# Kernel tuning notes

Measured on AMD Instinct MI355X. Metric: run time of the kernel, lower is better.

Reference implementation:

```python
import jax, jax.numpy as jnp
import numpy as np

N_NODES = 100000

def _spmm(edge_index, edge_weight, support):
    # out[dst] += w * support[src]  == sparse adj @ support
    src, dst = edge_index[0], edge_index[1]
    msgs = support[src] * edge_weight[:, None]
    return jax.ops.segment_sum(msgs, dst, num_segments=N_NODES)


def setup_inputs() -> dict:
    key = jax.random.key(0)
    k1, k2, k3, k4, k5 = jax.random.split(key, 5)
    n_feat, n_hid, n_class = 512, 256, 40
    E = 3200000
    x = jax.random.normal(k1, (N_NODES, n_feat), dtype=jnp.float32)
    edge_index = jax.random.randint(k2, (2, E), 0, N_NODES, dtype=jnp.int64)
    edge_weight = jax.random.uniform(k3, (E,), dtype=jnp.float32)
    # Xavier-uniform-like init
    lim1 = float(np.sqrt(6.0 / (n_feat + n_hid)))
    lim2 = float(np.sqrt(6.0 / (n_hid + n_class)))
    W1 = jax.random.uniform(k4, (n_feat, n_hid), minval=-lim1, maxval=lim1, dtype=jnp.float32)
    W2 = jax.random.uniform(k5, (n_hid, n_class), minval=-lim2, maxval=lim2, dtype=jnp.float32)
    return {"x": x, "edge_index": edge_index, "edge_weight": edge_weight, "W1": W1, "W2": W2}


def reference(x, edge_index, edge_weight, W1, W2):
    # layer 1: dense projection then sparse aggregation, relu
    h = jax.nn.relu(_spmm(edge_index, edge_weight, x @ W1))
    # dropout is identity in eval mode (deterministic reference)
    # layer 2
    logits = _spmm(edge_index, edge_weight, h @ W2)
    return jax.nn.log_softmax(logits, axis=1)
```

## Files before the change

kernel.cpp:

```cpp
#include <hip/hip_runtime.h>
#include <math.h>

#define N_FEAT 512
#define F_HID  256
#define F_OUT  40
#define P_STRIDE 64

#define NBLK1 128
#define CAP   224

typedef unsigned short u16;
typedef unsigned int   u32;
typedef unsigned char  u8;
typedef __attribute__((ext_vector_type(8))) short bf8_t;
typedef __attribute__((ext_vector_type(4))) float f32x4;
typedef __attribute__((ext_vector_type(2))) float f32x2;

__device__ __forceinline__ u16 f2bf(float f) {
    unsigned u = __float_as_uint(f);
    u += 0x7FFFu + ((u >> 16) & 1u);
    return (u16)(u >> 16);
}
__device__ __forceinline__ float bf2f(u16 h) {
    return __uint_as_float(((unsigned)h) << 16);
}
__device__ __forceinline__ float bfLo(u32 u) { return __uint_as_float(u << 16); }
__device__ __forceinline__ float bfHi(u32 u) { return __uint_as_float(u & 0xFFFF0000u); }

__global__ void prep_weights(const float* __restrict__ W1, const float* __restrict__ W2,
                             u16* __restrict__ W1T, u16* __restrict__ W2T) {
    int idx = blockIdx.x * blockDim.x + threadIdx.x;
    if (idx < F_HID * N_FEAT) {
        int n = idx >> 9, k = idx & 511;
        W1T[idx] = f2bf(W1[k * F_HID + n]);
    }
    int idx2 = idx - F_HID * N_FEAT;
    if (idx2 >= 0 && idx2 < 48 * 256) {
        int n = idx2 >> 8, k = idx2 & 255;
        W2T[idx2] = (n < F_OUT) ? f2bf(W2[k * F_OUT + n]) : (u16)0;
    }
}

__global__ __launch_bounds__(256) void bucket_kernel(const int* __restrict__ src,
                                                     const int* __restrict__ dst,
                                                     const float* __restrict__ w,
                                                     int2* __restrict__ region,
                                                     int* __restrict__ cnt_g,
                                                     int E, int NB) {
    __shared__ int cnt[256];
    int tid = threadIdx.x;
    cnt[tid] = 0;
    __syncthreads();
    int2* myreg = region + (size_t)blockIdx.x * NB * CAP;
    for (int i = blockIdx.x * 256 + tid; i < E; i += NBLK1 * 256) {
        int d = dst[i];
        int b = d >> 9;
        int pos = atomicAdd(&cnt[b], 1);
        if (pos < CAP)
            myreg[(size_t)b * CAP + pos] =
                make_int2((d & 511) | (src[i] << 9), __float_as_int(w[i]));
    }
    __syncthreads();
    if (tid < NB) cnt_g[blockIdx.x * NB + tid] = min(cnt[tid], CAP);
}

__global__ __launch_bounds__(256) void bucket_scan(const int* __restrict__ cnt_g,
                                                   int* __restrict__ Bb, int NB) {
    __shared__ int t[256];
    int tid = threadIdx.x;
    int T = 0;
    if (tid < NB)
        for (int blk = 0; blk < NBLK1; ++blk) T += cnt_g[blk * NB + tid];
    t[tid] = T;
    __syncthreads();
    for (int d = 1; d < 256; d <<= 1) {
        int v = (tid >= d) ? t[tid - d] : 0;
        __syncthreads();
        t[tid] += v;
        __syncthreads();
    }
    if (tid < NB) Bb[tid] = t[tid] - T;
}

__global__ __launch_bounds__(256) void build_csr(const int2* __restrict__ region,
                                                 const int* __restrict__ cnt_g,
                                                 const int* __restrict__ Bb,
                                                 int* __restrict__ deg,
                                                 int* __restrict__ offs,
                                                 int2* __restrict__ edges,
                                                 int M, int NB) {
    int b = blockIdx.x, tid = threadIdx.x;
    __shared__ int hist[512], excl[512], curi[512], pc[NBLK1];
    __shared__ int s1[256];
    hist[tid] = 0; hist[tid + 256] = 0;
    for (int t = tid; t < NBLK1; t += 256) pc[t] = cnt_g[t * NB + b];
    __syncthreads();
    for (int blk = 0; blk < NBLK1; ++blk) {
        int n = pc[blk];
        const int2* rp = region + ((size_t)blk * NB + b) * CAP;
        for (int j = tid; j < n; j += 256)
            atomicAdd(&hist[rp[j].x & 511], 1);
    }
    __syncthreads();
    int h0 = hist[2 * tid], h1 = hist[2 * tid + 1];
    s1[tid] = h0 + h1;
    __syncthreads();
    for (int d = 1; d < 256; d <<= 1) {
        int v = (tid >= d) ? s1[tid - d] : 0;
        __syncthreads();
        s1[tid] += v;
        __syncthreads();
    }
    int ex = s1[tid] - (h0 + h1);
    excl[2 * tid] = ex;       excl[2 * tid + 1] = ex + h0;
    curi[2 * tid] = ex;       curi[2 * tid + 1] = ex + h0;
    __syncthreads();
    int base = Bb[b];
    for (int t = tid; t < 512; t += 256) {
        int d = b * 512 + t;
        if (d < M) { deg[d] = hist[t]; offs[d] = base + excl[t]; }
    }
    for (int blk = 0; blk < NBLK1; ++blk) {
        int n = pc[blk];
        const int2* rp = region + ((size_t)blk * NB + b) * CAP;
        for (int j = tid; j < n; j += 256) {
            int2 e = rp[j];
            int ld = e.x & 511;
            int p = atomicAdd(&curi[ld], 1);
            edges[base + p] = make_int2(e.x >> 9, e.y);
        }
    }
}

__global__ __launch_bounds__(256) void gemm1_kernel(const float* __restrict__ X,
                                                    const u16* __restrict__ W1T,
                                                    u8* __restrict__ H0, int M) {
    __shared__ float As[2][2048];
    int tid  = threadIdx.x;
    int wv   = tid >> 6, lane = tid & 63;
    int l15  = lane & 15, quad = lane >> 4;
    int m0   = blockIdx.x * 64;

    int p16_0 = wv * 64 + lane;
    int p16_1 = 256 + wv * 64 + lane;
    int r0 = p16_0 >> 3, sc0 = (p16_0 & 7) ^ (r0 & 7);
    int r1 = p16_1 >> 3, sc1 = (p16_1 & 7) ^ (r1 & 7);
    const float* src0 = X + (size_t)min(m0 + r0, M - 1) * N_FEAT + sc0 * 4;
    const float* src1 = X + (size_t)min(m0 + r1, M - 1) * N_FEAT + sc1 * 4;

    f32x4 acc[4][4] = {};

    auto stage = [&](int c, int buf) {
        __builtin_amdgcn_global_load_lds(
            (const __attribute__((address_space(1))) void*)(src0 + c * 32),
            (__attribute__((address_space(3))) void*)(&As[buf][wv * 256]), 16, 0, 0);
        __builtin_amdgcn_global_load_lds(
            (const __attribute__((address_space(1))) void*)(src1 + c * 32),
            (__attribute__((address_space(3))) void*)(&As[buf][1024 + wv * 256]), 16, 0, 0);
    };

    stage(0, 0);
    __syncthreads();
    for (int c = 0; c < 16; ++c) {
        int cur = c & 1;
        if (c + 1 < 16) stage(c + 1, cur ^ 1);
        bf8_t b[4];
#pragma unroll
        for (int nt = 0; nt < 4; ++nt)
            b[nt] = *(const bf8_t*)(W1T + (size_t)(wv * 64 + nt * 16 + l15) * N_FEAT + c * 32 + quad * 8);
#pragma unroll
        for (int mt = 0; mt < 4; ++mt) {
            int m = mt * 16 + l15;
            int scA = (quad * 2) ^ (m & 7);
            int scB = (quad * 2 + 1) ^ (m & 7);
            f32x4 x0 = *(const f32x4*)(&As[cur][m * 32 + scA * 4]);
            f32x4 x1 = *(const f32x4*)(&As[cur][m * 32 + scB * 4]);
            bf8_t a;
            a[0] = (short)f2bf(x0[0]); a[1] = (short)f2bf(x0[1]);
            a[2] = (short)f2bf(x0[2]); a[3] = (short)f2bf(x0[3]);
            a[4] = (short)f2bf(x1[0]); a[5] = (short)f2bf(x1[1]);
            a[6] = (short)f2bf(x1[2]); a[7] = (short)f2bf(x1[3]);
#pragma unroll
            for (int nt = 0; nt < 4; ++nt)
                acc[mt][nt] = __builtin_amdgcn_mfma_f32_16x16x32_bf16(a, b[nt], acc[mt][nt], 0, 0, 0);
        }
        __syncthreads();
    }
#pragma unroll
    for (int mt = 0; mt < 4; ++mt)
#pragma unroll
        for (int nt = 0; nt < 4; ++nt)
#pragma unroll
            for (int r = 0; r < 4; ++r) {
                int row = m0 + mt * 16 + quad * 4 + r;
                if (row < M) {
                    int pk = __builtin_amdgcn_cvt_pk_fp8_f32(acc[mt][nt][r], 0.f, 0, false);
                    H0[(size_t)row * F_HID + wv * 64 + nt * 16 + l15] = (u8)(pk & 0xFF);
                }
            }
}

__global__ __launch_bounds__(256) void spmm1_kernel(const u8* __restrict__ H0,
                                                    const int* __restrict__ offs,
                                                    const int* __restrict__ deg,
                                                    const int2* __restrict__ edges,
                                                    u16* __restrict__ H1, int M) {
    __shared__ int2 sE[4][64];
    int wv = threadIdx.x >> 6, lane = threadIdx.x & 63;
    int d = blockIdx.x * 4 + wv;
    if (d >= M) return;
    int start = offs[d], cnt = deg[d];
    int q = lane >> 4, l16 = lane & 15;
    const u8* hp = H0 + l16 * 16;
    float acc[16] = {};
    for (int base = 0; base < cnt; base += 64) {
        int c = min(64, cnt - base);
        int2 ev = make_int2(0, 0);
        if (lane < c) ev = edges[start + base + lane];
        sE[wv][lane] = ev;
        int jt = (c + 31) >> 5;
        for (int j = 0; j < jt; ++j) {
            int2 e[8];
#pragma unroll
            for (int k = 0; k < 8; ++k)
                e[k] = sE[wv][32 * j + 4 * k + q];
            uint4 v[8];
#pragma unroll
            for (int k = 0; k < 8; ++k)
                v[k] = *(const uint4*)(hp + (size_t)e[k].x * F_HID);
#pragma unroll
            for (int k = 0; k < 8; ++k) {
                float w = __int_as_float(e[k].y);
                u32 wd[4] = {v[k].x, v[k].y, v[k].z, v[k].w};
#pragma unroll
                for (int t = 0; t < 4; ++t) {
                    f32x2 lo = __builtin_amdgcn_cvt_pk_f32_fp8((int)wd[t], false);
                    f32x2 hi = __builtin_amdgcn_cvt_pk_f32_fp8((int)wd[t], true);
                    acc[4 * t + 0] = fmaf(w, lo[0], acc[4 * t + 0]);
                    acc[4 * t + 1] = fmaf(w, lo[1], acc[4 * t + 1]);
                    acc[4 * t + 2] = fmaf(w, hi[0], acc[4 * t + 2]);
                    acc[4 * t + 3] = fmaf(w, hi[1], acc[4 * t + 3]);
                }
            }
        }
    }
#pragma unroll
    for (int t = 0; t < 16; ++t) {
        acc[t] += __shfl_xor(acc[t], 16);
        acc[t] += __shfl_xor(acc[t], 32);
    }
    if (q == 0) {
        u16 o[16];
#pragma unroll
        for (int t = 0; t < 16; ++t) o[t] = f2bf(fmaxf(acc[t], 0.f));
        uint4 r0, r1;
        r0.x = (u32)o[0]  | ((u32)o[1]  << 16);
        r0.y = (u32)o[2]  | ((u32)o[3]  << 16);
        r0.z = (u32)o[4]  | ((u32)o[5]  << 16);
        r0.w = (u32)o[6]  | ((u32)o[7]  << 16);
        r1.x = (u32)o[8]  | ((u32)o[9]  << 16);
        r1.y = (u32)o[10] | ((u32)o[11] << 16);
        r1.z = (u32)o[12] | ((u32)o[13] << 16);
        r1.w = (u32)o[14] | ((u32)o[15] << 16);
        uint4* dst16 = (uint4*)(H1 + (size_t)d * F_HID + l16 * 16);
        dst16[0] = r0;
        dst16[1] = r1;
    }
}

__global__ __launch_bounds__(256) void gemm2_kernel(const u16* __restrict__ H1,
                                                    const u16* __restrict__ W2T,
                                                    u16* __restrict__ P, int M) {
    __shared__ u16 Bs[2][8192];
    int tid  = threadIdx.x;
    int wv   = tid >> 6, lane = tid & 63;
    int l15  = lane & 15, quad = lane >> 4;
    int m0   = blockIdx.x * 128;

    f32x4 acc[2][3] = {};

    auto stage = [&](int c, int buf) {
#pragma unroll
        for (int jj = 0; jj < 4; ++jj) {
            int p16 = jj * 256 + wv * 64 + lane;
            int r   = p16 >> 3;
            int sc  = (p16 & 7) ^ (r & 7);
            const u16* src = H1 + (size_t)min(m0 + r, M - 1) * F_HID + c * 64 + sc * 8;
            __builtin_amdgcn_global_load_lds(
                (const __attribute__((address_space(1))) void*)src,
                (__attribute__((address_space(3))) void*)(&Bs[buf][jj * 2048 + wv * 512]), 16, 0, 0);
        }
    };

    stage(0, 0);
    __syncthreads();
    for (int c = 0; c < 4; ++c) {
        int cur = c & 1;
        if (c + 1 < 4) stage(c + 1, cur ^ 1);
#pragma unroll
        for (int ks = 0; ks < 2; ++ks) {
            bf8_t b[3];
#pragma unroll
            for (int nt = 0; nt < 3; ++nt)
                b[nt] = *(const bf8_t*)(W2T + (size_t)(nt * 16 + l15) * F_HID + c * 64 + ks * 32 + quad * 8);
#pragma unroll
            for (int mt = 0; mt < 2; ++mt) {
                int m  = wv * 32 + mt * 16 + l15;
                int sc = (ks * 4 + quad) ^ (m & 7);
                bf8_t a = *(const bf8_t*)(&Bs[cur][m * 64 + sc * 8]);
#pragma unroll
                for (int nt = 0; nt < 3; ++nt)
                    acc[mt][nt] = __builtin_amdgcn_mfma_f32_16x16x32_bf16(a, b[nt], acc[mt][nt], 0, 0, 0);
            }
        }
        __syncthreads();
    }
#pragma unroll
    for (int mt = 0; mt < 2; ++mt)
#pragma unroll
        for (int nt = 0; nt < 3; ++nt)
#pragma unroll
            for (int r = 0; r < 4; ++r) {
                int row = m0 + wv * 32 + mt * 16 + quad * 4 + r;
                int col = nt * 16 + l15;
                if (row < M && col < F_OUT)
                    P[(size_t)row * P_STRIDE + col] = f2bf(acc[mt][nt][r]);
            }
}

__global__ __launch_bounds__(256) void spmm2_kernel(const u16* __restrict__ P,
                                                    const int* __restrict__ offs,
                                                    const int* __restrict__ deg,
                                                    const int2* __restrict__ edges,
                                                    float* __restrict__ out, int M) {
    __shared__ int2 sE[4][64];
    int wv = threadIdx.x >> 6, lane = threadIdx.x & 63;
    int d = blockIdx.x * 4 + wv;
    if (d >= M) return;
    int start = offs[d], cnt = deg[d];
    int q = lane >> 4, l16 = lane & 15;
    const u16* pp = P + l16 * 4;
    float acc[4] = {};
    for (int base = 0; base < cnt; base += 64) {
        int c = min(64, cnt - base);
        int2 ev = make_int2(0, 0);
        if (lane < c) ev = edges[start + base + lane];
        sE[wv][lane] = ev;
        int jt = (c + 31) >> 5;
        for (int j = 0; j < jt; ++j) {
            int2 e[8];
#pragma unroll
            for (int k = 0; k < 8; ++k)
                e[k] = sE[wv][32 * j + 4 * k + q];
            uint2 v[8];
#pragma unroll
            for (int k = 0; k < 8; ++k)
                v[k] = *(const uint2*)(pp + (size_t)e[k].x * P_STRIDE);
#pragma unroll
            for (int k = 0; k < 8; ++k) {
                float w = __int_as_float(e[k].y);
                acc[0] = fmaf(w, bfLo(v[k].x), acc[0]); acc[1] = fmaf(w, bfHi(v[k].x), acc[1]);
                acc[2] = fmaf(w, bfLo(v[k].y), acc[2]); acc[3] = fmaf(w, bfHi(v[k].y), acc[3]);
            }
        }
    }
#pragma unroll
    for (int t = 0; t < 4; ++t) {
        acc[t] += __shfl_xor(acc[t], 16);
        acc[t] += __shfl_xor(acc[t], 32);
    }
    int fbase = l16 * 4;
    float mx = -INFINITY;
#pragma unroll
    for (int t = 0; t < 4; ++t)
        if (fbase + t < F_OUT) mx = fmaxf(mx, acc[t]);
#pragma unroll
    for (int off = 8; off >= 1; off >>= 1) mx = fmaxf(mx, __shfl_xor(mx, off));
    float sm = 0.f;
#pragma unroll
    for (int t = 0; t < 4; ++t)
        if (fbase + t < F_OUT) sm += expf(acc[t] - mx);
#pragma unroll
    for (int off = 8; off >= 1; off >>= 1) sm += __shfl_xor(sm, off);
    if (q == 0 && l16 < 10) {
        float lse = mx + logf(sm);
        f32x4 o;
#pragma unroll
        for (int t = 0; t < 4; ++t) o[t] = acc[t] - lse;
        *(f32x4*)(out + (size_t)d * F_OUT + fbase) = o;
    }
}

extern "C" void kernel_launch(void* const* d_in, const int* in_sizes, int n_in,
                              void* d_out, int out_size, void* d_ws, size_t ws_size,
                              hipStream_t stream) {
    const float* x   = (const float*)d_in[0];
    const int*   eix = (const int*)d_in[1];
    const float* ewt = (const float*)d_in[2];
    const float* W1  = (const float*)d_in[3];
    const float* W2  = (const float*)d_in[4];
    float* out = (float*)d_out;

    const int E = in_sizes[2];
    const int M = out_size / F_OUT;
    const int NB = (M + 511) >> 9;
    const int* src = eix;
    const int* dst = eix + E;

    char* ws = (char*)d_ws;
    size_t off = 0;
    auto take = [&](size_t bytes) -> void* {
        void* p = ws + off;
        off = (off + bytes + 255) & ~(size_t)255;
        return p;
    };
    u8*    H0     = (u8*)take((size_t)M * F_HID * sizeof(u8));
    u16*   H1     = (u16*)take((size_t)M * F_HID * sizeof(u16));
    u16*   W1T    = (u16*)take((size_t)F_HID * N_FEAT * sizeof(u16));
    u16*   W2T    = (u16*)take((size_t)48 * 256 * sizeof(u16));
    u16*   P      = (u16*)take((size_t)M * P_STRIDE * sizeof(u16));
    int*   deg    = (int*)take((size_t)M * sizeof(int));
    int*   offs   = (int*)take((size_t)M * sizeof(int));
    int*   Bb     = (int*)take(256 * sizeof(int));
    int*   cnt_g  = (int*)take((size_t)NBLK1 * NB * sizeof(int));
    int2*  edges  = (int2*)take((size_t)E * sizeof(int2));
    int2*  region = (int2*)take((size_t)NBLK1 * NB * CAP * sizeof(int2));
    (void)ws_size; (void)n_in;

    int prep_n = F_HID * N_FEAT + 48 * 256;
    prep_weights<<<(prep_n + 255) / 256, 256, 0, stream>>>(W1, W2, W1T, W2T);

    bucket_kernel<<<NBLK1, 256, 0, stream>>>(src, dst, ewt, region, cnt_g, E, NB);
    bucket_scan<<<1, 256, 0, stream>>>(cnt_g, Bb, NB);
    build_csr<<<NB, 256, 0, stream>>>(region, cnt_g, Bb, deg, offs, edges, M, NB);

    gemm1_kernel<<<(M + 63) / 64, 256, 0, stream>>>(x, W1T, H0, M);
    spmm1_kernel<<<(M + 3) / 4, 256, 0, stream>>>(H0, offs, deg, edges, H1, M);
    gemm2_kernel<<<(M + 127) / 128, 256, 0, stream>>>(H1, W2T, P, M);
    spmm2_kernel<<<(M + 3) / 4, 256, 0, stream>>>(P, offs, deg, edges, out, M);
}
```

Baseline: 732.6 us.

## Build CSR via global atomics count-scan-scatter and store layer-2 projection as fp8

Replaces the capped bucket-region CSR build with a global degree count, a multi-block prefix scan, and an atomic-cursor scatter. This removes the per-block capacity limit and the large region buffer, but issues global atomics on random destinations and leaves edge order within each row nondeterministic. The layer-2 projection P is stored as fp8 instead of bf16, halving gather bytes in spmm2. spmm2 is remapped so 8 lanes each cover 8 features, with tail-edge guards added to both spmm kernels.

```diff
diff --git a/kernel.cpp b/kernel.cpp
--- a/kernel.cpp
+++ b/kernel.cpp
@@ -4,10 +4,6 @@
 #define N_FEAT 512
 #define F_HID  256
 #define F_OUT  40
-#define P_STRIDE 64
-
-#define NBLK1 128
-#define CAP   224
 
 typedef unsigned short u16;
 typedef unsigned int   u32;
@@ -21,14 +17,12 @@
     u += 0x7FFFu + ((u >> 16) & 1u);
     return (u16)(u >> 16);
 }
-__device__ __forceinline__ float bf2f(u16 h) {
-    return __uint_as_float(((unsigned)h) << 16);
-}
 __device__ __forceinline__ float bfLo(u32 u) { return __uint_as_float(u << 16); }
 __device__ __forceinline__ float bfHi(u32 u) { return __uint_as_float(u & 0xFFFF0000u); }
 
 __global__ void prep_weights(const float* __restrict__ W1, const float* __restrict__ W2,
-                             u16* __restrict__ W1T, u16* __restrict__ W2T) {
+                             u16* __restrict__ W1T, u16* __restrict__ W2T,
+                             int* __restrict__ deg, int M) {
     int idx = blockIdx.x * blockDim.x + threadIdx.x;
     if (idx < F_HID * N_FEAT) {
         int n = idx >> 9, k = idx & 511;
@@ -39,96 +33,79 @@
         int n = idx2 >> 8, k = idx2 & 255;
         W2T[idx2] = (n < F_OUT) ? f2bf(W2[k * F_OUT + n]) : (u16)0;
     }
-}
-
-__global__ __launch_bounds__(256) void bucket_kernel(const int* __restrict__ src,
-                                                     const int* __restrict__ dst,
-                                                     const float* __restrict__ w,
-                                                     int2* __restrict__ region,
-                                                     int* __restrict__ cnt_g,
-                                                     int E, int NB) {
-    __shared__ int cnt[256];
-    int tid = threadIdx.x;
-    cnt[tid] = 0;
-    __syncthreads();
-    int2* myreg = region + (size_t)blockIdx.x * NB * CAP;
-    for (int i = blockIdx.x * 256 + tid; i < E; i += NBLK1 * 256) {
-        int d = dst[i];
-        int b = d >> 9;
-        int pos = atomicAdd(&cnt[b], 1);
-        if (pos < CAP)
-            myreg[(size_t)b * CAP + pos] =
-                make_int2((d & 511) | (src[i] << 9), __float_as_int(w[i]));
-    }
-    __syncthreads();
-    if (tid < NB) cnt_g[blockIdx.x * NB + tid] = min(cnt[tid], CAP);
-}
-
-__global__ __launch_bounds__(256) void bucket_scan(const int* __restrict__ cnt_g,
-                                                   int* __restrict__ Bb, int NB) {
+    if (idx < M) deg[idx] = 0;
+}
+
+__global__ __launch_bounds__(256) void count_kernel(const int* __restrict__ dst,
+                                                    int* __restrict__ deg, int E) {
+    int i = blockIdx.x * 256 + threadIdx.x;
+    int stride = gridDim.x * 256;
+    for (; i < E; i += stride) atomicAdd(&deg[dst[i]], 1);
+}
+
+__global__ __launch_bounds__(256) void scan_bsum(const int* __restrict__ deg,
+                                                 int* __restrict__ bsum, int M) {
+    __shared__ int s[256];
+    int b = blockIdx.x, tid = threadIdx.x;
+    int i0 = b * 512;
+    int v = 0;
+    if (i0 + tid < M) v += deg[i0 + tid];
+    if (i0 + 256 + tid < M) v += deg[i0 + 256 + tid];
+    s[tid] = v; __syncthreads();
+    for (int d = 128; d > 0; d >>= 1) {
+        if (tid < d) s[tid] += s[tid + d];
+        __syncthreads();
+    }
+    if (tid == 0) bsum[b] = s[0];
+}
+
+__global__ __launch_bounds__(256) void scan_bbase(const int* __restrict__ bsum,
+                                                  int* __restrict__ bbase, int NB) {
     __shared__ int t[256];
     int tid = threadIdx.x;
-    int T = 0;
-    if (tid < NB)
-        for (int blk = 0; blk < NBLK1; ++blk) T += cnt_g[blk * NB + tid];
-    t[tid] = T;
-    __syncthreads();
+    int v = (tid < NB) ? bsum[tid] : 0;
+    t[tid] = v; __syncthreads();
     for (int d = 1; d < 256; d <<= 1) {
-        int v = (tid >= d) ? t[tid - d] : 0;
-        __syncthreads();
-        t[tid] += v;
-        __syncthreads();
-    }
-    if (tid < NB) Bb[tid] = t[tid] - T;
-}
-
-__global__ __launch_bounds__(256) void build_csr(const int2* __restrict__ region,
-                                                 const int* __restrict__ cnt_g,
-                                                 const int* __restrict__ Bb,
-                                                 int* __restrict__ deg,
+        int u = (tid >= d) ? t[tid - d] : 0;
+        __syncthreads();
+        t[tid] += u;
+        __syncthreads();
+    }
+    if (tid < NB) bbase[tid] = t[tid] - v;
+}
+
+__global__ __launch_bounds__(256) void scan_offs(const int* __restrict__ deg,
+                                                 const int* __restrict__ bbase,
                                                  int* __restrict__ offs,
-                                                 int2* __restrict__ edges,
-                                                 int M, int NB) {
+                                                 int* __restrict__ cursor, int M) {
+    __shared__ int s1[256];
     int b = blockIdx.x, tid = threadIdx.x;
-    __shared__ int hist[512], excl[512], curi[512], pc[NBLK1];
-    __shared__ int s1[256];
-    hist[tid] = 0; hist[tid + 256] = 0;
-    for (int t = tid; t < NBLK1; t += 256) pc[t] = cnt_g[t * NB + b];
-    __syncthreads();
-    for (int blk = 0; blk < NBLK1; ++blk) {
-        int n = pc[blk];
-        const int2* rp = region + ((size_t)blk * NB + b) * CAP;
-        for (int j = tid; j < n; j += 256)
-            atomicAdd(&hist[rp[j].x & 511], 1);
-    }
-    __syncthreads();
-    int h0 = hist[2 * tid], h1 = hist[2 * tid + 1];
-    s1[tid] = h0 + h1;
-    __syncthreads();
+    int i0 = b * 512;
+    int d0 = (i0 + 2 * tid < M) ? deg[i0 + 2 * tid] : 0;
+    int d1 = (i0 + 2 * tid + 1 < M) ? deg[i0 + 2 * tid + 1] : 0;
+    s1[tid] = d0 + d1; __syncthreads();
     for (int d = 1; d < 256; d <<= 1) {
-        int v = (tid >= d) ? s1[tid - d] : 0;
-        __syncthreads();
-        s1[tid] += v;
-        __syncthreads();
-    }
-    int ex = s1[tid] - (h0 + h1);
-    excl[2 * tid] = ex;       excl[2 * tid + 1] = ex + h0;
-    curi[2 * tid] = ex;       curi[2 * tid + 1] = ex + h0;
-    __syncthreads();
-    int base = Bb[b];
-    for (int t = tid; t < 512; t += 256) {
-        int d = b * 512 + t;
-        if (d < M) { deg[d] = hist[t]; offs[d] = base + excl[t]; }
-    }
-    for (int blk = 0; blk < NBLK1; ++blk) {
-        int n = pc[blk];
-        const int2* rp = region + ((size_t)blk * NB + b) * CAP;
-        for (int j = tid; j < n; j += 256) {
-            int2 e = rp[j];
-            int ld = e.x & 511;
-            int p = atomicAdd(&curi[ld], 1);
-            edges[base + p] = make_int2(e.x >> 9, e.y);
-        }
+        int u = (tid >= d) ? s1[tid - d] : 0;
+        __syncthreads();
+        s1[tid] += u;
+        __syncthreads();
+    }
+    int ex = s1[tid] - (d0 + d1) + bbase[b];
+    if (i0 + 2 * tid < M)     { offs[i0 + 2 * tid] = ex;      cursor[i0 + 2 * tid] = ex; }
+    if (i0 + 2 * tid + 1 < M) { offs[i0 + 2 * tid + 1] = ex + d0; cursor[i0 + 2 * tid + 1] = ex + d0; }
+}
+
+__global__ __launch_bounds__(256) void scatter_kernel(const int* __restrict__ src,
+                                                      const int* __restrict__ dst,
+                                                      const float* __restrict__ w,
+                                                      int* __restrict__ cursor,
+                                                      int2* __restrict__ edges, int E) {
+    int i = blockIdx.x * 256 + threadIdx.x;
+    int stride = gridDim.x * 256;
+    for (; i < E; i += stride) {
+        int d = dst[i];
+        int p = atomicAdd(&cursor[d], 1);
+        edges[p] = make_int2(src[i], __float_as_int(w[i]));
     }
 }
 
@@ -230,16 +207,18 @@
                 v[k] = *(const uint4*)(hp + (size_t)e[k].x * F_HID);
 #pragma unroll
             for (int k = 0; k < 8; ++k) {
-                float w = __int_as_float(e[k].y);
-                u32 wd[4] = {v[k].x, v[k].y, v[k].z, v[k].w};
-#pragma unroll
-                for (int t = 0; t < 4; ++t) {
-                    f32x2 lo = __builtin_amdgcn_cvt_pk_f32_fp8((int)wd[t], false);
-                    f32x2 hi = __builtin_amdgcn_cvt_pk_f32_fp8((int)wd[t], true);
-                    acc[4 * t + 0] = fmaf(w, lo[0], acc[4 * t + 0]);
-                    acc[4 * t + 1] = fmaf(w, lo[1], acc[4 * t + 1]);
-                    acc[4 * t + 2] = fmaf(w, hi[0], acc[4 * t + 2]);
-                    acc[4 * t + 3] = fmaf(w, hi[1], acc[4 * t + 3]);
+                if (32 * j + 4 * k < c) {
+                    float w = __int_as_float(e[k].y);
+                    u32 wd[4] = {v[k].x, v[k].y, v[k].z, v[k].w};
+#pragma unroll
+                    for (int t = 0; t < 4; ++t) {
+                        f32x2 lo = __builtin_amdgcn_cvt_pk_f32_fp8((int)wd[t], false);
+                        f32x2 hi = __builtin_amdgcn_cvt_pk_f32_fp8((int)wd[t], true);
+                        acc[4 * t + 0] = fmaf(w, lo[0], acc[4 * t + 0]);
+                        acc[4 * t + 1] = fmaf(w, lo[1], acc[4 * t + 1]);
+                        acc[4 * t + 2] = fmaf(w, hi[0], acc[4 * t + 2]);
+                        acc[4 * t + 3] = fmaf(w, hi[1], acc[4 * t + 3]);
+                    }
                 }
             }
         }
@@ -270,7 +249,7 @@
 
 __global__ __launch_bounds__(256) void gemm2_kernel(const u16* __restrict__ H1,
                                                     const u16* __restrict__ W2T,
-                                                    u16* __restrict__ P, int M) {
+                                                    u8* __restrict__ P, int M) {
     __shared__ u16 Bs[2][8192];
     int tid  = threadIdx.x;
     int wv   = tid >> 6, lane = tid & 63;
@@ -323,12 +302,22 @@
             for (int r = 0; r < 4; ++r) {
                 int row = m0 + wv * 32 + mt * 16 + quad * 4 + r;
                 int col = nt * 16 + l15;
-                if (row < M && col < F_OUT)
-                    P[(size_t)row * P_STRIDE + col] = f2bf(acc[mt][nt][r]);
+                if (row < M) {
+                    u8 val = 0;
+                    if (col < F_OUT) {
+                        int pk = __builtin_amdgcn_cvt_pk_fp8_f32(acc[mt][nt][r], 0.f, 0, false);
+                        val = (u8)(pk & 0xFF);
+                    }
+                    P[(size_t)row * 64 + col] = val;
+                }
             }
-}
-
-__global__ __launch_bounds__(256) void spmm2_kernel(const u16* __restrict__ P,
+    for (int rr = tid; rr < 128; rr += 256) {
+        int row = m0 + rr;
+        if (row < M) *(uint4*)(P + (size_t)row * 64 + 48) = make_uint4(0, 0, 0, 0);
+    }
+}
+
+__global__ __launch_bounds__(256) void spmm2_kernel(const u8* __restrict__ P,
                                                     const int* __restrict__ offs,
                                                     const int* __restrict__ deg,
                                                     const int2* __restrict__ edges,
@@ -338,56 +327,65 @@
     int d = blockIdx.x * 4 + wv;
     if (d >= M) return;
     int start = offs[d], cnt = deg[d];
-    int q = lane >> 4, l16 = lane & 15;
-    const u16* pp = P + l16 * 4;
-    float acc[4] = {};
+    int g = lane >> 3, l8 = lane & 7;
+    const u8* pp = P + l8 * 8;
+    float acc[8] = {};
     for (int base = 0; base < cnt; base += 64) {
         int c = min(64, cnt - base);
         int2 ev = make_int2(0, 0);
         if (lane < c) ev = edges[start + base + lane];
         sE[wv][lane] = ev;
-        int jt = (c + 31) >> 5;
-        for (int j = 0; j < jt; ++j) {
-            int2 e[8];
-#pragma unroll
-            for (int k = 0; k < 8; ++k)
-                e[k] = sE[wv][32 * j + 4 * k + q];
-            uint2 v[8];
-#pragma unroll
-            for (int k = 0; k < 8; ++k)
-                v[k] = *(const uint2*)(pp + (size_t)e[k].x * P_STRIDE);
-#pragma unroll
-            for (int k = 0; k < 8; ++k) {
+        int2 e[8];
+#pragma unroll
+        for (int k = 0; k < 8; ++k)
+            e[k] = sE[wv][8 * k + g];
+        uint2 v[8];
+#pragma unroll
+        for (int k = 0; k < 8; ++k)
+            v[k] = *(const uint2*)(pp + (size_t)e[k].x * 64);
+#pragma unroll
+        for (int k = 0; k < 8; ++k) {
+            if (8 * k < c) {
                 float w = __int_as_float(e[k].y);
-                acc[0] = fmaf(w, bfLo(v[k].x), acc[0]); acc[1] = fmaf(w, bfHi(v[k].x), acc[1]);
-                acc[2] = fmaf(w, bfLo(v[k].y), acc[2]); acc[3] = fmaf(w, bfHi(v[k].y), acc[3]);
+                f32x2 lo0 = __builtin_amdgcn_cvt_pk_f32_fp8((int)v[k].x, false);
+                f32x2 hi0 = __builtin_amdgcn_cvt_pk_f32_fp8((int)v[k].x, true);
+                f32x2 lo1 = __builtin_amdgcn_cvt_pk_f32_fp8((int)v[k].y, false);
+                f32x2 hi1 = __builtin_amdgcn_cvt_pk_f32_fp8((int)v[k].y, true);
+                acc[0] = fmaf(w, lo0[0], acc[0]); acc[1] = fmaf(w, lo0[1], acc[1]);
+                acc[2] = fmaf(w, hi0[0], acc[2]); acc[3] = fmaf(w, hi0[1], acc[3]);
+                acc[4] = fmaf(w, lo1[0], acc[4]); acc[5] = fmaf(w, lo1[1], acc[5]);
+                acc[6] = fmaf(w, hi1[0], acc[6]); acc[7] = fmaf(w, hi1[1], acc[7]);
             }
         }
     }
 #pragma unroll
-    for (int t = 0; t < 4; ++t) {
+    for (int t = 0; t < 8; ++t) {
+        acc[t] += __shfl_xor(acc[t], 8);
         acc[t] += __shfl_xor(acc[t], 16);
         acc[t] += __shfl_xor(acc[t], 32);
     }
-    int fbase = l16 * 4;
     float mx = -INFINITY;
-#pragma unroll
-    for (int t = 0; t < 4; ++t)
-        if (fbase + t < F_OUT) mx = fmaxf(mx, acc[t]);
-#pragma unroll
-    for (int off = 8; off >= 1; off >>= 1) mx = fmaxf(mx, __shfl_xor(mx, off));
+    if (l8 < 5) {
+#pragma unroll
+        for (int t = 0; t < 8; ++t) mx = fmaxf(mx, acc[t]);
+    }
+#pragma unroll
+    for (int off = 4; off >= 1; off >>= 1) mx = fmaxf(mx, __shfl_xor(mx, off));
     float sm = 0.f;
-#pragma unroll
-    for (int t = 0; t < 4; ++t)
-        if (fbase + t < F_OUT) sm += expf(acc[t] - mx);
-#pragma unroll
-    for (int off = 8; off >= 1; off >>= 1) sm += __shfl_xor(sm, off);
-    if (q == 0 && l16 < 10) {
+    if (l8 < 5) {
+#pragma unroll
+        for (int t = 0; t < 8; ++t) sm += expf(acc[t] - mx);
+    }
+#pragma unroll
+    for (int off = 4; off >= 1; off >>= 1) sm += __shfl_xor(sm, off);
+    if (g == 0 && l8 < 5) {
         float lse = mx + logf(sm);
-        f32x4 o;
-#pragma unroll
-        for (int t = 0; t < 4; ++t) o[t] = acc[t] - lse;
-        *(f32x4*)(out + (size_t)d * F_OUT + fbase) = o;
+        f32x4 o0, o1;
+#pragma unroll
+        for (int t = 0; t < 4; ++t) { o0[t] = acc[t] - lse; o1[t] = acc[4 + t] - lse; }
+        f32x4* op = (f32x4*)(out + (size_t)d * F_OUT + l8 * 8);
+        op[0] = o0;
+        op[1] = o1;
     }
 }
 
@@ -418,21 +416,24 @@
     u16*   H1     = (u16*)take((size_t)M * F_HID * sizeof(u16));
     u16*   W1T    = (u16*)take((size_t)F_HID * N_FEAT * sizeof(u16));
     u16*   W2T    = (u16*)take((size_t)48 * 256 * sizeof(u16));
-    u16*   P      = (u16*)take((size_t)M * P_STRIDE * sizeof(u16));
+    u8*    P      = (u8*)take((size_t)M * 64 * sizeof(u8));
     int*   deg    = (int*)take((size_t)M * sizeof(int));
     int*   offs   = (int*)take((size_t)M * sizeof(int));
-    int*   Bb     = (int*)take(256 * sizeof(int));
-    int*   cnt_g  = (int*)take((size_t)NBLK1 * NB * sizeof(int));
+    int*   cursor = (int*)take((size_t)M * sizeof(int));
+    int*   bsum   = (int*)take(256 * sizeof(int));
+    int*   bbase  = (int*)take(256 * sizeof(int));
     int2*  edges  = (int2*)take((size_t)E * sizeof(int2));
-    int2*  region = (int2*)take((size_t)NBLK1 * NB * CAP * sizeof(int2));
     (void)ws_size; (void)n_in;
 
     int prep_n = F_HID * N_FEAT + 48 * 256;
-    prep_weights<<<(prep_n + 255) / 256, 256, 0, stream>>>(W1, W2, W1T, W2T);
-
-    bucket_kernel<<<NBLK1, 256, 0, stream>>>(src, dst, ewt, region, cnt_g, E, NB);
-    bucket_scan<<<1, 256, 0, stream>>>(cnt_g, Bb, NB);
-    build_csr<<<NB, 256, 0, stream>>>(region, cnt_g, Bb, deg, offs, edges, M, NB);
+    int prep_grid = (max(prep_n, M) + 255) / 256;
+    prep_weights<<<prep_grid, 256, 0, stream>>>(W1, W2, W1T, W2T, deg, M);
+
+    count_kernel<<<2048, 256, 0, stream>>>(dst, deg, E);
+    scan_bsum<<<NB, 256, 0, stream>>>(deg, bsum, M);
+    scan_bbase<<<1, 256, 0, stream>>>(bsum, bbase, NB);
+    scan_offs<<<NB, 256, 0, stream>>>(deg, bbase, offs, cursor, M);
+    scatter_kernel<<<2048, 256, 0, stream>>>(src, dst, ewt, cursor, edges, E);
 
     gemm1_kernel<<<(M + 63) / 64, 256, 0, stream>>>(x, W1T, H0, M);
     spmm1_kernel<<<(M + 3) / 4, 256, 0, stream>>>(H0, offs, deg, edges, H1, M);
```

Measured after the change: 911.1 us. 24.4% more time.

## Store layer-2 projection as FP8 and regroup SpMM2 gather lanes

Applied to the files above, without the earlier changes.

The gemm2 output P moves from bf16 at stride 64 to fp8 at stride 64 bytes. This halves the bytes gathered per edge in spmm2, which now maps 8 lanes × 8 features so each wave processes 8 edges per step instead of 4. The spmm1 and spmm2 inner loops also skip FMAs for padded edge slots beyond the chunk count. The trade-off is more quantization error in the logits before log_softmax, plus a byte-wise scattered store in gemm2.

```diff
diff --git a/kernel.cpp b/kernel.cpp
--- a/kernel.cpp
+++ b/kernel.cpp
@@ -4,7 +4,6 @@
 #define N_FEAT 512
 #define F_HID  256
 #define F_OUT  40
-#define P_STRIDE 64
 
 #define NBLK1 128
 #define CAP   224
@@ -20,9 +19,6 @@
     unsigned u = __float_as_uint(f);
     u += 0x7FFFu + ((u >> 16) & 1u);
     return (u16)(u >> 16);
-}
-__device__ __forceinline__ float bf2f(u16 h) {
-    return __uint_as_float(((unsigned)h) << 16);
 }
 __device__ __forceinline__ float bfLo(u32 u) { return __uint_as_float(u << 16); }
 __device__ __forceinline__ float bfHi(u32 u) { return __uint_as_float(u & 0xFFFF0000u); }
@@ -230,16 +226,18 @@
                 v[k] = *(const uint4*)(hp + (size_t)e[k].x * F_HID);
 #pragma unroll
             for (int k = 0; k < 8; ++k) {
-                float w = __int_as_float(e[k].y);
-                u32 wd[4] = {v[k].x, v[k].y, v[k].z, v[k].w};
-#pragma unroll
-                for (int t = 0; t < 4; ++t) {
-                    f32x2 lo = __builtin_amdgcn_cvt_pk_f32_fp8((int)wd[t], false);
-                    f32x2 hi = __builtin_amdgcn_cvt_pk_f32_fp8((int)wd[t], true);
-                    acc[4 * t + 0] = fmaf(w, lo[0], acc[4 * t + 0]);
-                    acc[4 * t + 1] = fmaf(w, lo[1], acc[4 * t + 1]);
-                    acc[4 * t + 2] = fmaf(w, hi[0], acc[4 * t + 2]);
-                    acc[4 * t + 3] = fmaf(w, hi[1], acc[4 * t + 3]);
+                if (32 * j + 4 * k < c) {
+                    float w = __int_as_float(e[k].y);
+                    u32 wd[4] = {v[k].x, v[k].y, v[k].z, v[k].w};
+#pragma unroll
+                    for (int t = 0; t < 4; ++t) {
+                        f32x2 lo = __builtin_amdgcn_cvt_pk_f32_fp8((int)wd[t], false);
+                        f32x2 hi = __builtin_amdgcn_cvt_pk_f32_fp8((int)wd[t], true);
+                        acc[4 * t + 0] = fmaf(w, lo[0], acc[4 * t + 0]);
+                        acc[4 * t + 1] = fmaf(w, lo[1], acc[4 * t + 1]);
+                        acc[4 * t + 2] = fmaf(w, hi[0], acc[4 * t + 2]);
+                        acc[4 * t + 3] = fmaf(w, hi[1], acc[4 * t + 3]);
+                    }
                 }
             }
         }
@@ -270,7 +268,7 @@
 
 __global__ __launch_bounds__(256) void gemm2_kernel(const u16* __restrict__ H1,
                                                     const u16* __restrict__ W2T,
-                                                    u16* __restrict__ P, int M) {
+                                                    u8* __restrict__ P, int M) {
     __shared__ u16 Bs[2][8192];
     int tid  = threadIdx.x;
     int wv   = tid >> 6, lane = tid & 63;
@@ -323,12 +321,22 @@
             for (int r = 0; r < 4; ++r) {
                 int row = m0 + wv * 32 + mt * 16 + quad * 4 + r;
                 int col = nt * 16 + l15;
-                if (row < M && col < F_OUT)
-                    P[(size_t)row * P_STRIDE + col] = f2bf(acc[mt][nt][r]);
+                if (row < M) {
+                    u8 val = 0;
+                    if (col < F_OUT) {
+                        int pk = __builtin_amdgcn_cvt_pk_fp8_f32(acc[mt][nt][r], 0.f, 0, false);
+                        val = (u8)(pk & 0xFF);
+                    }
+                    P[(size_t)row * 64 + col] = val;
+                }
             }
-}
-
-__global__ __launch_bounds__(256) void spmm2_kernel(const u16* __restrict__ P,
+    for (int rr = tid; rr < 128; rr += 256) {
+        int row = m0 + rr;
+        if (row < M) *(uint4*)(P + (size_t)row * 64 + 48) = make_uint4(0, 0, 0, 0);
+    }
+}
+
+__global__ __launch_bounds__(256) void spmm2_kernel(const u8* __restrict__ P,
                                                     const int* __restrict__ offs,
                                                     const int* __restrict__ deg,
                                                     const int2* __restrict__ edges,
@@ -338,56 +346,65 @@
     int d = blockIdx.x * 4 + wv;
     if (d >= M) return;
     int start = offs[d], cnt = deg[d];
-    int q = lane >> 4, l16 = lane & 15;
-    const u16* pp = P + l16 * 4;
-    float acc[4] = {};
+    int g = lane >> 3, l8 = lane & 7;
+    const u8* pp = P + l8 * 8;
+    float acc[8] = {};
     for (int base = 0; base < cnt; base += 64) {
         int c = min(64, cnt - base);
         int2 ev = make_int2(0, 0);
         if (lane < c) ev = edges[start + base + lane];
         sE[wv][lane] = ev;
-        int jt = (c + 31) >> 5;
-        for (int j = 0; j < jt; ++j) {
-            int2 e[8];
-#pragma unroll
-            for (int k = 0; k < 8; ++k)
-                e[k] = sE[wv][32 * j + 4 * k + q];
-            uint2 v[8];
-#pragma unroll
-            for (int k = 0; k < 8; ++k)
-                v[k] = *(const uint2*)(pp + (size_t)e[k].x * P_STRIDE);
-#pragma unroll
-            for (int k = 0; k < 8; ++k) {
+        int2 e[8];
+#pragma unroll
+        for (int k = 0; k < 8; ++k)
+            e[k] = sE[wv][8 * k + g];
+        uint2 v[8];
+#pragma unroll
+        for (int k = 0; k < 8; ++k)
+            v[k] = *(const uint2*)(pp + (size_t)e[k].x * 64);
+#pragma unroll
+        for (int k = 0; k < 8; ++k) {
+            if (8 * k < c) {
                 float w = __int_as_float(e[k].y);
-                acc[0] = fmaf(w, bfLo(v[k].x), acc[0]); acc[1] = fmaf(w, bfHi(v[k].x), acc[1]);
-                acc[2] = fmaf(w, bfLo(v[k].y), acc[2]); acc[3] = fmaf(w, bfHi(v[k].y), acc[3]);
+                f32x2 lo0 = __builtin_amdgcn_cvt_pk_f32_fp8((int)v[k].x, false);
+                f32x2 hi0 = __builtin_amdgcn_cvt_pk_f32_fp8((int)v[k].x, true);
+                f32x2 lo1 = __builtin_amdgcn_cvt_pk_f32_fp8((int)v[k].y, false);
+                f32x2 hi1 = __builtin_amdgcn_cvt_pk_f32_fp8((int)v[k].y, true);
+                acc[0] = fmaf(w, lo0[0], acc[0]); acc[1] = fmaf(w, lo0[1], acc[1]);
+                acc[2] = fmaf(w, hi0[0], acc[2]); acc[3] = fmaf(w, hi0[1], acc[3]);
+                acc[4] = fmaf(w, lo1[0], acc[4]); acc[5] = fmaf(w, lo1[1], acc[5]);
+                acc[6] = fmaf(w, hi1[0], acc[6]); acc[7] = fmaf(w, hi1[1], acc[7]);
             }
         }
     }
 #pragma unroll
-    for (int t = 0; t < 4; ++t) {
+    for (int t = 0; t < 8; ++t) {
+        acc[t] += __shfl_xor(acc[t], 8);
         acc[t] += __shfl_xor(acc[t], 16);
         acc[t] += __shfl_xor(acc[t], 32);
     }
-    int fbase = l16 * 4;
     float mx = -INFINITY;
-#pragma unroll
-    for (int t = 0; t < 4; ++t)
-        if (fbase + t < F_OUT) mx = fmaxf(mx, acc[t]);
-#pragma unroll
-    for (int off = 8; off >= 1; off >>= 1) mx = fmaxf(mx, __shfl_xor(mx, off));
+    if (l8 < 5) {
+#pragma unroll
+        for (int t = 0; t < 8; ++t) mx = fmaxf(mx, acc[t]);
+    }
+#pragma unroll
+    for (int off = 4; off >= 1; off >>= 1) mx = fmaxf(mx, __shfl_xor(mx, off));
     float sm = 0.f;
-#pragma unroll
-    for (int t = 0; t < 4; ++t)
-        if (fbase + t < F_OUT) sm += expf(acc[t] - mx);
-#pragma unroll
-    for (int off = 8; off >= 1; off >>= 1) sm += __shfl_xor(sm, off);
-    if (q == 0 && l16 < 10) {
+    if (l8 < 5) {
+#pragma unroll
+        for (int t = 0; t < 8; ++t) sm += expf(acc[t] - mx);
+    }
+#pragma unroll
+    for (int off = 4; off >= 1; off >>= 1) sm += __shfl_xor(sm, off);
+    if (g == 0 && l8 < 5) {
         float lse = mx + logf(sm);
-        f32x4 o;
-#pragma unroll
-        for (int t = 0; t < 4; ++t) o[t] = acc[t] - lse;
-        *(f32x4*)(out + (size_t)d * F_OUT + fbase) = o;
+        f32x4 o0, o1;
+#pragma unroll
+        for (int t = 0; t < 4; ++t) { o0[t] = acc[t] - lse; o1[t] = acc[4 + t] - lse; }
+        f32x4* op = (f32x4*)(out + (size_t)d * F_OUT + l8 * 8);
+        op[0] = o0;
+        op[1] = o1;
     }
 }
 
@@ -418,7 +435,7 @@
     u16*   H1     = (u16*)take((size_t)M * F_HID * sizeof(u16));
     u16*   W1T    = (u16*)take((size_t)F_HID * N_FEAT * sizeof(u16));
     u16*   W2T    = (u16*)take((size_t)48 * 256 * sizeof(u16));
-    u16*   P      = (u16*)take((size_t)M * P_STRIDE * sizeof(u16));
+    u8*    P      = (u8*)take((size_t)M * 64 * sizeof(u8));
     int*   deg    = (int*)take((size_t)M * sizeof(int));
     int*   offs   = (int*)take((size_t)M * sizeof(int));
     int*   Bb     = (int*)take(256 * sizeof(int));
```

Measured after the change: 714.8 us. -2.4%, faster.
